# Kernel tuning notes

Measured on AMD Instinct MI355X. Metric: run time of the kernel, lower is better.

Reference implementation:

```python
import jax, jax.numpy as jnp
import numpy as np

B, H, N, D = 2, 16, 2048, 128

def setup_inputs() -> dict:
    key = jax.random.key(0)
    kq, kk, kv = jax.random.split(key, 3)
    q = jax.random.normal(kq, (B, H, N, D), dtype=jnp.float32)
    k = jax.random.normal(kk, (B, H, N, D), dtype=jnp.float32)
    v = jax.random.normal(kv, (B, H, N, D), dtype=jnp.float32)
    return {"q": q, "k": k, "v": v}

def reference(q, k, v):
    # scale = 1/sqrt(d) computed at forward time (scale=None in __init__)
    d = q.shape[-1]
    scale = 1.0 / jnp.sqrt(jnp.asarray(d, dtype=q.dtype))
    # scores: (B, H, N, N)
    scores = jnp.einsum('bhnd,bhmd->bhnm', q, k) * scale
    probs = jax.nn.softmax(scores, axis=-1)
    return jnp.einsum('bhnm,bhmd->bhnd', probs, v)
```

## Files before the change

kernel.cpp:

```cpp
#include <hip/hip_runtime.h>
#include <hip/hip_fp16.h>

#define BH   32
#define SEQ  2048
#define DIM  128
#define CK   32
#define NCH  (SEQ / CK)

typedef _Float16 half8   __attribute__((ext_vector_type(8)));
typedef __fp16   fp16x2  __attribute__((ext_vector_type(2)));
typedef _Float16 half2v  __attribute__((ext_vector_type(2)));
typedef float    floatx4 __attribute__((ext_vector_type(4)));

__device__ inline half2v pk2(float a, float b) {
    fp16x2 t = __builtin_amdgcn_cvt_pkrtz(a, b);
    return *(half2v*)&t;
}
__device__ inline half8 pk8(float4 a, float4 b) {
    half2v l0 = pk2(a.x, a.y), l1 = pk2(a.z, a.w);
    half2v l2 = pk2(b.x, b.y), l3 = pk2(b.z, b.w);
    half8 h;
    h[0] = l0[0]; h[1] = l0[1]; h[2] = l1[0]; h[3] = l1[1];
    h[4] = l2[0]; h[5] = l2[1]; h[6] = l3[0]; h[7] = l3[1];
    return h;
}

__device__ inline void ld16(const void* g, void* l) {
    __builtin_amdgcn_global_load_lds(
        (__attribute__((address_space(1))) void*)(uintptr_t)g,
        (__attribute__((address_space(3))) void*)(uintptr_t)l, 16, 0, 0);
}

#define SYNC_VM(N) do {                                        \
    asm volatile("s_waitcnt vmcnt(" #N ")" ::: "memory");      \
    __builtin_amdgcn_s_barrier();                              \
    asm volatile("" ::: "memory");                             \
} while (0)

__global__ void prep_kernel(const float* __restrict__ k, const float* __restrict__ v,
                            _Float16* __restrict__ kh, _Float16* __restrict__ vt) {
    const float SC = 0.08838834764831845f * 1.4426950408889634f;
    __shared__ __align__(16) _Float16 t[32][136];
    const int bh = blockIdx.x >> 6;
    const int kc = blockIdx.x & 63;
    const int tid = threadIdx.x;
    const size_t base = ((size_t)bh * SEQ + kc * CK) * DIM;

    const float4* kf4 = (const float4*)(k + base);
    const float4* vf4 = (const float4*)(v + base);
    half8* kh8 = (half8*)(kh + base);

    #pragma unroll
    for (int i = 0; i < 2; i++) {
        int f8 = i * 256 + tid;
        float4 a = kf4[2 * f8], b = kf4[2 * f8 + 1];
        a.x *= SC; a.y *= SC; a.z *= SC; a.w *= SC;
        b.x *= SC; b.y *= SC; b.z *= SC; b.w *= SC;
        kh8[f8] = pk8(a, b);
        int row = f8 >> 4, c8 = f8 & 15;
        *((half8*)&t[row][c8 * 8]) = pk8(vf4[2 * f8], vf4[2 * f8 + 1]);
    }
    __syncthreads();
    _Float16* vout = vt + ((size_t)bh * NCH + kc) * (DIM * CK);
    #pragma unroll
    for (int i = 0; i < 2; i++) {
        int g = i * 256 + tid;
        int d = g >> 2, kg = g & 3;
        half8 h;
        #pragma unroll
        for (int j = 0; j < 8; j++) h[j] = t[kg * 8 + j][d];
        *((half8*)(vout + d * CK + kg * 8)) = h;
    }
}

__global__ __launch_bounds__(256, 2) void attn_kernel(
        const float* __restrict__ q, const _Float16* __restrict__ kh,
        const _Float16* __restrict__ vt, float* __restrict__ out) {
    __shared__ __align__(16) _Float16 Kbuf[3][CK * DIM];
    __shared__ __align__(16) _Float16 Vbuf[4][DIM * CK];
    __shared__ __align__(16) _Float16 Pld[4][2][16][40];

    const int lid = blockIdx.x + (blockIdx.y << 4);
    const int xcd = lid & 7;
    const int idx = lid >> 3;
    const int bh  = (xcd << 2) + (idx >> 4);
    const int qt  = idx & 15;

    const int tid  = threadIdx.x;
    const int w    = tid >> 6;
    const int lane = tid & 63;
    const int l15  = lane & 15;
    const int quad = lane >> 4;

    {
        float4 z4 = {0.f, 0.f, 0.f, 0.f};
        ((float4*)&Vbuf[3][0])[tid] = z4;
        ((float4*)&Vbuf[3][0])[tid + 256] = z4;
        asm volatile("s_waitcnt lgkmcnt(0)" ::: "memory");
    }

    half8 qf[2][4];
    #pragma unroll
    for (int s = 0; s < 2; s++) {
        const float* qb = q + ((size_t)bh * SEQ + qt * 128 + w * 32 + s * 16 + l15) * DIM;
        #pragma unroll
        for (int c = 0; c < 4; c++) {
            float4 a = *((const float4*)(qb + c * 32 + quad * 8));
            float4 b = *((const float4*)(qb + c * 32 + quad * 8 + 4));
            qf[s][c] = pk8(a, b);
        }
    }

    half8 ones;
    #pragma unroll
    for (int j = 0; j < 8; j++) ones[j] = (_Float16)1.0f;

    floatx4 zf = {0.f, 0.f, 0.f, 0.f};
    floatx4 O[2][8];
    #pragma unroll
    for (int s = 0; s < 2; s++)
        #pragma unroll
        for (int i = 0; i < 8; i++) O[s][i] = zf;
    floatx4 Osum[2] = {zf, zf};

    const _Float16* kb = kh + (size_t)bh * SEQ * DIM;
    const _Float16* vb = vt + (size_t)bh * SEQ * DIM;

    const int s0 = w * 128 + lane;
    const int s1 = s0 + 64;
    const int kr0 = s0 >> 4, kg0 = ((s0 & 15) - 3 * (kr0 >> 1)) & 15;
    const int kr1 = s1 >> 4, kg1 = ((s1 & 15) - 3 * (kr1 >> 1)) & 15;
    const _Float16* kgp0 = kb + kr0 * DIM + kg0 * 8;
    const _Float16* kgp1 = kb + kr1 * DIM + kg1 * 8;
    const int vo0 = ((s0 >> 6) * 16 + (s0 & 15)) * CK + ((s0 >> 4) & 3) * 8;
    const int vo1 = ((s1 >> 6) * 16 + (s1 & 15)) * CK + ((s1 >> 4) & 3) * 8;
    const _Float16* vgp0 = vb + vo0;
    const _Float16* vgp1 = vb + vo1;

    auto dma = [&](int kc, int bk, int bv) {
        size_t off = (size_t)kc * (CK * DIM);
        ld16(kgp0 + off, &Kbuf[bk][(w * 2 + 0) * 512]);
        ld16(kgp1 + off, &Kbuf[bk][(w * 2 + 1) * 512]);
        ld16(vgp0 + off, &Vbuf[bv][(w * 2 + 0) * 512]);
        ld16(vgp1 + off, &Vbuf[bv][(w * 2 + 1) * 512]);
    };

    const int row0 = 2 * l15, row1 = 2 * l15 + 1;

    half8 pf0, pf1;
    #pragma unroll
    for (int j = 0; j < 8; j++) { pf0[j] = (_Float16)0.0f; pf1[j] = (_Float16)0.0f; }

    dma(0, 0, 0);
    dma(1, 1, 1);

    int bk = 0;
    #pragma unroll 3
    for (int kc = 0; kc < NCH - 1; kc++) {
        SYNC_VM(4);
        if (kc + 2 < NCH) {
            int bk2 = bk + 2; if (bk2 >= 3) bk2 -= 3;
            dma(kc + 2, bk2, (kc + 2) & 3);
        }

        const _Float16* Kc = Kbuf[bk];

        floatx4 S[2][2];
        #pragma unroll
        for (int s = 0; s < 2; s++) { S[s][0] = zf; S[s][1] = zf; }
        __builtin_amdgcn_s_setprio(1);
        #pragma unroll
        for (int c = 0; c < 4; c++) {
            int P = ((c * 4 + quad) + 3 * l15) & 15;
            half8 b0 = *((const half8*)&Kc[row0 * DIM + P * 8]);
            half8 b1 = *((const half8*)&Kc[row1 * DIM + P * 8]);
            #pragma unroll
            for (int s = 0; s < 2; s++) {
                S[s][0] = __builtin_amdgcn_mfma_f32_16x16x32_f16(qf[s][c], b0, S[s][0], 0, 0, 0);
                S[s][1] = __builtin_amdgcn_mfma_f32_16x16x32_f16(qf[s][c], b1, S[s][1], 0, 0, 0);
            }
        }
        __builtin_amdgcn_s_setprio(0);

        const _Float16* Vp = Vbuf[(kc + 3) & 3];
        half8 vfr[8];
        #pragma unroll
        for (int dt = 0; dt < 8; dt++)
            vfr[dt] = *((const half8*)&Vp[dt * 512 + (quad * 16 + l15) * 8]);

        #pragma unroll
        for (int s = 0; s < 2; s++)
            #pragma unroll
            for (int r = 0; r < 4; r++) {
                float p0 = __builtin_amdgcn_exp2f(S[s][0][r]);
                float p1 = __builtin_amdgcn_exp2f(S[s][1][r]);
                *((half2v*)&Pld[w][s][quad * 4 + r][2 * l15]) = pk2(p0, p1);
            }

        __builtin_amdgcn_s_setprio(1);
        Osum[0] = __builtin_amdgcn_mfma_f32_16x16x32_f16(pf0, ones, Osum[0], 0, 0, 0);
        Osum[1] = __builtin_amdgcn_mfma_f32_16x16x32_f16(pf1, ones, Osum[1], 0, 0, 0);
        #pragma unroll
        for (int dt = 0; dt < 8; dt++) {
            O[0][dt] = __builtin_amdgcn_mfma_f32_16x16x32_f16(pf0, vfr[dt], O[0][dt], 0, 0, 0);
            O[1][dt] = __builtin_amdgcn_mfma_f32_16x16x32_f16(pf1, vfr[dt], O[1][dt], 0, 0, 0);
        }
        __builtin_amdgcn_s_setprio(0);

        pf0 = *((const half8*)&Pld[w][0][l15][quad * 8]);
        pf1 = *((const half8*)&Pld[w][1][l15][quad * 8]);

        bk++; if (bk == 3) bk = 0;
    }

    SYNC_VM(0);
    {
        const _Float16* Kc = Kbuf[bk];
        floatx4 S[2][2];
        #pragma unroll
        for (int s = 0; s < 2; s++) { S[s][0] = zf; S[s][1] = zf; }
        __builtin_amdgcn_s_setprio(1);
        #pragma unroll
        for (int c = 0; c < 4; c++) {
            int P = ((c * 4 + quad) + 3 * l15) & 15;
            half8 b0 = *((const half8*)&Kc[row0 * DIM + P * 8]);
            half8 b1 = *((const half8*)&Kc[row1 * DIM + P * 8]);
            #pragma unroll
            for (int s = 0; s < 2; s++) {
                S[s][0] = __builtin_amdgcn_mfma_f32_16x16x32_f16(qf[s][c], b0, S[s][0], 0, 0, 0);
                S[s][1] = __builtin_amdgcn_mfma_f32_16x16x32_f16(qf[s][c], b1, S[s][1], 0, 0, 0);
            }
        }
        __builtin_amdgcn_s_setprio(0);

        const _Float16* Vp = Vbuf[(NCH + 2) & 3];
        half8 vfr[8];
        #pragma unroll
        for (int dt = 0; dt < 8; dt++)
            vfr[dt] = *((const half8*)&Vp[dt * 512 + (quad * 16 + l15) * 8]);

        #pragma unroll
        for (int s = 0; s < 2; s++)
            #pragma unroll
            for (int r = 0; r < 4; r++) {
                float p0 = __builtin_amdgcn_exp2f(S[s][0][r]);
                float p1 = __builtin_amdgcn_exp2f(S[s][1][r]);
                *((half2v*)&Pld[w][s][quad * 4 + r][2 * l15]) = pk2(p0, p1);
            }

        __builtin_amdgcn_s_setprio(1);
        Osum[0] = __builtin_amdgcn_mfma_f32_16x16x32_f16(pf0, ones, Osum[0], 0, 0, 0);
        Osum[1] = __builtin_amdgcn_mfma_f32_16x16x32_f16(pf1, ones, Osum[1], 0, 0, 0);
        #pragma unroll
        for (int dt = 0; dt < 8; dt++) {
            O[0][dt] = __builtin_amdgcn_mfma_f32_16x16x32_f16(pf0, vfr[dt], O[0][dt], 0, 0, 0);
            O[1][dt] = __builtin_amdgcn_mfma_f32_16x16x32_f16(pf1, vfr[dt], O[1][dt], 0, 0, 0);
        }
        __builtin_amdgcn_s_setprio(0);

        pf0 = *((const half8*)&Pld[w][0][l15][quad * 8]);
        pf1 = *((const half8*)&Pld[w][1][l15][quad * 8]);

        const _Float16* Vl = Vbuf[(NCH - 1) & 3];
        half8 vfl[8];
        #pragma unroll
        for (int dt = 0; dt < 8; dt++)
            vfl[dt] = *((const half8*)&Vl[dt * 512 + (quad * 16 + l15) * 8]);
        __builtin_amdgcn_s_setprio(1);
        Osum[0] = __builtin_amdgcn_mfma_f32_16x16x32_f16(pf0, ones, Osum[0], 0, 0, 0);
        Osum[1] = __builtin_amdgcn_mfma_f32_16x16x32_f16(pf1, ones, Osum[1], 0, 0, 0);
        #pragma unroll
        for (int dt = 0; dt < 8; dt++) {
            O[0][dt] = __builtin_amdgcn_mfma_f32_16x16x32_f16(pf0, vfl[dt], O[0][dt], 0, 0, 0);
            O[1][dt] = __builtin_amdgcn_mfma_f32_16x16x32_f16(pf1, vfl[dt], O[1][dt], 0, 0, 0);
        }
        __builtin_amdgcn_s_setprio(0);
    }

    #pragma unroll
    for (int s = 0; s < 2; s++) {
        float* ob = out + ((size_t)bh * SEQ + qt * 128 + w * 32 + s * 16) * DIM;
        #pragma unroll
        for (int r = 0; r < 4; r++) {
            float rinv = 1.0f / Osum[s][r];
            #pragma unroll
            for (int dt = 0; dt < 8; dt++) {
                ob[(size_t)(quad * 4 + r) * DIM + dt * 16 + l15] = O[s][dt][r] * rinv;
            }
        }
    }
}

extern "C" void kernel_launch(void* const* d_in, const int* in_sizes, int n_in,
                              void* d_out, int out_size, void* d_ws, size_t ws_size,
                              hipStream_t stream) {
    const float* q = (const float*)d_in[0];
    const float* k = (const float*)d_in[1];
    const float* v = (const float*)d_in[2];
    float* out = (float*)d_out;

    const size_t elems = (size_t)BH * SEQ * DIM;
    _Float16* kh = (_Float16*)d_ws;
    _Float16* vtp = kh + elems;

    prep_kernel<<<BH * NCH, 256, 0, stream>>>(k, v, kh, vtp);
    attn_kernel<<<dim3(SEQ / 128, BH), 256, 0, stream>>>(q, kh, vtp, out);
}
```

Measured before the change: 203.0 us.

## Compute transposed S=K·Q so P stays in registers, drop LDS round-trip

Swaps the operand order of the QK^T MFMA so each lane's output directly forms the A-operand fragment of the PV MFMA. K rows are permuted during the global-to-LDS copy so the register layout matches. This removes the Pld shared-memory buffer and its per-iteration write/read. The main loop body is also factored into a lambda. The risk is that the key permutation must line up exactly with the V layout for the results to be correct.

```diff
diff --git a/kernel.cpp b/kernel.cpp
--- a/kernel.cpp
+++ b/kernel.cpp
@@ -78,7 +78,6 @@
         const _Float16* __restrict__ vt, float* __restrict__ out) {
     __shared__ __align__(16) _Float16 Kbuf[3][CK * DIM];
     __shared__ __align__(16) _Float16 Vbuf[4][DIM * CK];
-    __shared__ __align__(16) _Float16 Pld[4][2][16][40];
 
     const int lid = blockIdx.x + (blockIdx.y << 4);
     const int xcd = lid & 7;
@@ -128,28 +127,92 @@
 
     const int s0 = w * 128 + lane;
     const int s1 = s0 + 64;
-    const int kr0 = s0 >> 4, kg0 = ((s0 & 15) - 3 * (kr0 >> 1)) & 15;
-    const int kr1 = s1 >> 4, kg1 = ((s1 & 15) - 3 * (kr1 >> 1)) & 15;
-    const _Float16* kgp0 = kb + kr0 * DIM + kg0 * 8;
-    const _Float16* kgp1 = kb + kr1 * DIM + kg1 * 8;
+    const int rho0 = s0 >> 4, Pos0 = s0 & 15;
+    const int rho1 = s1 >> 4, Pos1 = s1 & 15;
+    const int g0 = (Pos0 - 3 * rho0) & 15;
+    const int g1 = (Pos1 - 3 * rho1) & 15;
+    const int key0 = (((rho0 >> 2) & 3) << 3) + ((rho0 >> 4) << 2) + (rho0 & 3);
+    const int key1 = (((rho1 >> 2) & 3) << 3) + ((rho1 >> 4) << 2) + (rho1 & 3);
+    const _Float16* kgp0 = kb + key0 * DIM + g0 * 8;
+    const _Float16* kgp1 = kb + key1 * DIM + g1 * 8;
     const int vo0 = ((s0 >> 6) * 16 + (s0 & 15)) * CK + ((s0 >> 4) & 3) * 8;
     const int vo1 = ((s1 >> 6) * 16 + (s1 & 15)) * CK + ((s1 >> 4) & 3) * 8;
     const _Float16* vgp0 = vb + vo0;
     const _Float16* vgp1 = vb + vo1;
 
-    auto dma = [&](int kc, int bk, int bv) {
+    auto dma = [&](int kc, int bk_, int bv_) {
         size_t off = (size_t)kc * (CK * DIM);
-        ld16(kgp0 + off, &Kbuf[bk][(w * 2 + 0) * 512]);
-        ld16(kgp1 + off, &Kbuf[bk][(w * 2 + 1) * 512]);
-        ld16(vgp0 + off, &Vbuf[bv][(w * 2 + 0) * 512]);
-        ld16(vgp1 + off, &Vbuf[bv][(w * 2 + 1) * 512]);
+        ld16(kgp0 + off, &Kbuf[bk_][(w * 2 + 0) * 512]);
+        ld16(kgp1 + off, &Kbuf[bk_][(w * 2 + 1) * 512]);
+        ld16(vgp0 + off, &Vbuf[bv_][(w * 2 + 0) * 512]);
+        ld16(vgp1 + off, &Vbuf[bv_][(w * 2 + 1) * 512]);
     };
 
-    const int row0 = 2 * l15, row1 = 2 * l15 + 1;
-
     half8 pf0, pf1;
     #pragma unroll
     for (int j = 0; j < 8; j++) { pf0[j] = (_Float16)0.0f; pf1[j] = (_Float16)0.0f; }
+
+    auto body = [&](int kc, int bk_) {
+        const _Float16* Kc = Kbuf[bk_];
+
+        floatx4 S[2][2];
+        #pragma unroll
+        for (int s = 0; s < 2; s++) { S[s][0] = zf; S[s][1] = zf; }
+        __builtin_amdgcn_s_setprio(1);
+        #pragma unroll
+        for (int c = 0; c < 4; c++) {
+            #pragma unroll
+            for (int j = 0; j < 2; j++) {
+                int rho = j * 16 + l15;
+                int Pos = (c * 4 + quad + 3 * rho) & 15;
+                half8 ka = *((const half8*)&Kc[rho * DIM + Pos * 8]);
+                S[0][j] = __builtin_amdgcn_mfma_f32_16x16x32_f16(ka, qf[0][c], S[0][j], 0, 0, 0);
+                S[1][j] = __builtin_amdgcn_mfma_f32_16x16x32_f16(ka, qf[1][c], S[1][j], 0, 0, 0);
+            }
+        }
+        __builtin_amdgcn_s_setprio(0);
+
+        const _Float16* Vp = Vbuf[(kc + 3) & 3];
+        half8 vfr[8];
+        #pragma unroll
+        for (int dt = 0; dt < 8; dt++)
+            vfr[dt] = *((const half8*)&Vp[dt * 512 + (quad * 16 + l15) * 8]);
+
+        half8 pn0, pn1;
+        {
+            float4 a, b;
+            a.x = __builtin_amdgcn_exp2f(S[0][0][0]);
+            a.y = __builtin_amdgcn_exp2f(S[0][0][1]);
+            a.z = __builtin_amdgcn_exp2f(S[0][0][2]);
+            a.w = __builtin_amdgcn_exp2f(S[0][0][3]);
+            b.x = __builtin_amdgcn_exp2f(S[0][1][0]);
+            b.y = __builtin_amdgcn_exp2f(S[0][1][1]);
+            b.z = __builtin_amdgcn_exp2f(S[0][1][2]);
+            b.w = __builtin_amdgcn_exp2f(S[0][1][3]);
+            pn0 = pk8(a, b);
+            a.x = __builtin_amdgcn_exp2f(S[1][0][0]);
+            a.y = __builtin_amdgcn_exp2f(S[1][0][1]);
+            a.z = __builtin_amdgcn_exp2f(S[1][0][2]);
+            a.w = __builtin_amdgcn_exp2f(S[1][0][3]);
+            b.x = __builtin_amdgcn_exp2f(S[1][1][0]);
+            b.y = __builtin_amdgcn_exp2f(S[1][1][1]);
+            b.z = __builtin_amdgcn_exp2f(S[1][1][2]);
+            b.w = __builtin_amdgcn_exp2f(S[1][1][3]);
+            pn1 = pk8(a, b);
+        }
+
+        __builtin_amdgcn_s_setprio(1);
+        Osum[0] = __builtin_amdgcn_mfma_f32_16x16x32_f16(pf0, ones, Osum[0], 0, 0, 0);
+        Osum[1] = __builtin_amdgcn_mfma_f32_16x16x32_f16(pf1, ones, Osum[1], 0, 0, 0);
+        #pragma unroll
+        for (int dt = 0; dt < 8; dt++) {
+            O[0][dt] = __builtin_amdgcn_mfma_f32_16x16x32_f16(pf0, vfr[dt], O[0][dt], 0, 0, 0);
+            O[1][dt] = __builtin_amdgcn_mfma_f32_16x16x32_f16(pf1, vfr[dt], O[1][dt], 0, 0, 0);
+        }
+        __builtin_amdgcn_s_setprio(0);
+
+        pf0 = pn0; pf1 = pn1;
+    };
 
     dma(0, 0, 0);
     dma(1, 1, 1);
@@ -162,105 +225,14 @@
             int bk2 = bk + 2; if (bk2 >= 3) bk2 -= 3;
             dma(kc + 2, bk2, (kc + 2) & 3);
         }
-
-        const _Float16* Kc = Kbuf[bk];
-
-        floatx4 S[2][2];
-        #pragma unroll
-        for (int s = 0; s < 2; s++) { S[s][0] = zf; S[s][1] = zf; }
-        __builtin_amdgcn_s_setprio(1);
-        #pragma unroll
-        for (int c = 0; c < 4; c++) {
-            int P = ((c * 4 + quad) + 3 * l15) & 15;
-            half8 b0 = *((const half8*)&Kc[row0 * DIM + P * 8]);
-            half8 b1 = *((const half8*)&Kc[row1 * DIM + P * 8]);
-            #pragma unroll
-            for (int s = 0; s < 2; s++) {
-                S[s][0] = __builtin_amdgcn_mfma_f32_16x16x32_f16(qf[s][c], b0, S[s][0], 0, 0, 0);
-                S[s][1] = __builtin_amdgcn_mfma_f32_16x16x32_f16(qf[s][c], b1, S[s][1], 0, 0, 0);
-            }
-        }
-        __builtin_amdgcn_s_setprio(0);
-
-        const _Float16* Vp = Vbuf[(kc + 3) & 3];
-        half8 vfr[8];
-        #pragma unroll
-        for (int dt = 0; dt < 8; dt++)
-            vfr[dt] = *((const half8*)&Vp[dt * 512 + (quad * 16 + l15) * 8]);
-
-        #pragma unroll
-        for (int s = 0; s < 2; s++)
-            #pragma unroll
-            for (int r = 0; r < 4; r++) {
-                float p0 = __builtin_amdgcn_exp2f(S[s][0][r]);
-                float p1 = __builtin_amdgcn_exp2f(S[s][1][r]);
-                *((half2v*)&Pld[w][s][quad * 4 + r][2 * l15]) = pk2(p0, p1);
-            }
-
-        __builtin_amdgcn_s_setprio(1);
-        Osum[0] = __builtin_amdgcn_mfma_f32_16x16x32_f16(pf0, ones, Osum[0], 0, 0, 0);
-        Osum[1] = __builtin_amdgcn_mfma_f32_16x16x32_f16(pf1, ones, Osum[1], 0, 0, 0);
-        #pragma unroll
-        for (int dt = 0; dt < 8; dt++) {
-            O[0][dt] = __builtin_amdgcn_mfma_f32_16x16x32_f16(pf0, vfr[dt], O[0][dt], 0, 0, 0);
-            O[1][dt] = __builtin_amdgcn_mfma_f32_16x16x32_f16(pf1, vfr[dt], O[1][dt], 0, 0, 0);
-        }
-        __builtin_amdgcn_s_setprio(0);
-
-        pf0 = *((const half8*)&Pld[w][0][l15][quad * 8]);
-        pf1 = *((const half8*)&Pld[w][1][l15][quad * 8]);
-
+        body(kc, bk);
         bk++; if (bk == 3) bk = 0;
     }
 
     SYNC_VM(0);
+    body(NCH - 1, bk);
+
     {
-        const _Float16* Kc = Kbuf[bk];
-        floatx4 S[2][2];
-        #pragma unroll
-        for (int s = 0; s < 2; s++) { S[s][0] = zf; S[s][1] = zf; }
-        __builtin_amdgcn_s_setprio(1);
-        #pragma unroll
-        for (int c = 0; c < 4; c++) {
-            int P = ((c * 4 + quad) + 3 * l15) & 15;
-            half8 b0 = *((const half8*)&Kc[row0 * DIM + P * 8]);
-            half8 b1 = *((const half8*)&Kc[row1 * DIM + P * 8]);
-            #pragma unroll
-            for (int s = 0; s < 2; s++) {
-                S[s][0] = __builtin_amdgcn_mfma_f32_16x16x32_f16(qf[s][c], b0, S[s][0], 0, 0, 0);
-                S[s][1] = __builtin_amdgcn_mfma_f32_16x16x32_f16(qf[s][c], b1, S[s][1], 0, 0, 0);
-            }
-        }
-        __builtin_amdgcn_s_setprio(0);
-
-        const _Float16* Vp = Vbuf[(NCH + 2) & 3];
-        half8 vfr[8];
-        #pragma unroll
-        for (int dt = 0; dt < 8; dt++)
-            vfr[dt] = *((const half8*)&Vp[dt * 512 + (quad * 16 + l15) * 8]);
-
-        #pragma unroll
-        for (int s = 0; s < 2; s++)
-            #pragma unroll
-            for (int r = 0; r < 4; r++) {
-                float p0 = __builtin_amdgcn_exp2f(S[s][0][r]);
-                float p1 = __builtin_amdgcn_exp2f(S[s][1][r]);
-                *((half2v*)&Pld[w][s][quad * 4 + r][2 * l15]) = pk2(p0, p1);
-            }
-
-        __builtin_amdgcn_s_setprio(1);
-        Osum[0] = __builtin_amdgcn_mfma_f32_16x16x32_f16(pf0, ones, Osum[0], 0, 0, 0);
-        Osum[1] = __builtin_amdgcn_mfma_f32_16x16x32_f16(pf1, ones, Osum[1], 0, 0, 0);
-        #pragma unroll
-        for (int dt = 0; dt < 8; dt++) {
-            O[0][dt] = __builtin_amdgcn_mfma_f32_16x16x32_f16(pf0, vfr[dt], O[0][dt], 0, 0, 0);
-            O[1][dt] = __builtin_amdgcn_mfma_f32_16x16x32_f16(pf1, vfr[dt], O[1][dt], 0, 0, 0);
-        }
-        __builtin_amdgcn_s_setprio(0);
-
-        pf0 = *((const half8*)&Pld[w][0][l15][quad * 8]);
-        pf1 = *((const half8*)&Pld[w][1][l15][quad * 8]);
-
         const _Float16* Vl = Vbuf[(NCH - 1) & 3];
         half8 vfl[8];
         #pragma unroll
```

New measurement: 199.2 us. About the same (-1.9%).
